# Kernel tuning notes

Measured on AMD Instinct MI355X. Metric: run time of the kernel, lower is better.

## Reference

```python
import jax, jax.numpy as jnp
import numpy as np

D_MODEL = 1024
D_STATE = 16
D_CONV = 4
EXPAND = 2
D_HALF = D_MODEL // 2            # per-direction model dim fed to each Mamba
D_INNER = EXPAND * D_HALF       # mamba inner dim
DT_RANK = (D_HALF + 15) // 16   # ceil(d_model/16), mamba default
EPS = 1e-5


def setup_inputs() -> dict:
    key = jax.random.key(0)
    ks = iter(jax.random.split(key, 64))

    def rn(shape, s=0.02):
        return jax.random.normal(next(ks), shape, dtype=jnp.float32) * s

    inp = {
        "x": jax.random.normal(next(ks), (2, 4096, D_MODEL), dtype=jnp.float32),
        "norm_w": jnp.ones((D_MODEL,), jnp.float32),
        "norm_b": jnp.zeros((D_MODEL,), jnp.float32),
    }
    for pre in ("fwd", "bwd"):
        inp[pre + "_in_proj_w"] = rn((2 * D_INNER, D_HALF))
        inp[pre + "_conv_w"] = rn((D_INNER, 1, D_CONV), 0.1)      # depthwise kernel
        inp[pre + "_conv_b"] = jnp.zeros((D_INNER,), jnp.float32)
        inp[pre + "_x_proj_w"] = rn((DT_RANK + 2 * D_STATE, D_INNER))
        inp[pre + "_dt_proj_w"] = rn((D_INNER, DT_RANK), 0.1)
        inp[pre + "_dt_proj_b"] = rn((D_INNER,), 0.1)
        # S4D-real init: A_log = log(1..d_state) broadcast over channels
        inp[pre + "_A_log"] = jnp.log(jnp.broadcast_to(
            jnp.arange(1, D_STATE + 1, dtype=jnp.float32), (D_INNER, D_STATE)))
        inp[pre + "_D"] = jnp.ones((D_INNER,), jnp.float32)
        inp[pre + "_out_proj_w"] = rn((D_HALF, D_INNER))
    return inp


def _silu(x):
    return x * jax.nn.sigmoid(x)


def _mamba(x, in_proj_w, conv_w, conv_b, x_proj_w, dt_proj_w, dt_proj_b,
           A_log, D, out_proj_w):
    # x: (B, L, D_HALF)
    B, L, _ = x.shape
    xz = x @ in_proj_w.T                         # (B, L, 2*D_INNER)
    xc, z = jnp.split(xz, 2, axis=-1)

    # causal depthwise conv over time
    xt = jnp.moveaxis(xc, 1, 2)                  # (B, D_INNER, L)
    xt = jnp.pad(xt, ((0, 0), (0, 0), (D_CONV - 1, 0)))
    xt = jax.lax.conv_general_dilated(
        xt, conv_w, (1,), 'VALID',
        dimension_numbers=('NCH', 'OIH', 'NCH'),
        feature_group_count=D_INNER)
    xc = _silu(jnp.moveaxis(xt, 1, 2) + conv_b)  # (B, L, D_INNER)

    x_dbl = xc @ x_proj_w.T                      # (B, L, DT_RANK + 2*D_STATE)
    dt = jax.nn.softplus(x_dbl[..., :DT_RANK] @ dt_proj_w.T + dt_proj_b)  # (B,L,D_INNER)
    Bm = x_dbl[..., DT_RANK:DT_RANK + D_STATE]   # (B, L, D_STATE)
    Cm = x_dbl[..., DT_RANK + D_STATE:]          # (B, L, D_STATE)
    A = -jnp.exp(A_log)                          # (D_INNER, D_STATE)

    def step(h, ins):
        dt_t, B_t, C_t, u_t = ins                # (B,D_INNER),(B,N),(B,N),(B,D_INNER)
        dA = jnp.exp(dt_t[..., None] * A)        # (B, D_INNER, N)
        h = h * dA + (dt_t * u_t)[..., None] * B_t[:, None, :]
        y = jnp.einsum('bdn,bn->bd', h, C_t)
        return h, y

    h0 = jnp.zeros((B, D_INNER, D_STATE), xc.dtype)
    ins = (jnp.moveaxis(dt, 1, 0), jnp.moveaxis(Bm, 1, 0),
           jnp.moveaxis(Cm, 1, 0), jnp.moveaxis(xc, 1, 0))
    _, ys = jax.lax.scan(step, h0, ins)          # ys: (L, B, D_INNER)
    y = jnp.moveaxis(ys, 0, 1) + D * xc
    y = y * _silu(z)
    return y @ out_proj_w.T                      # (B, L, D_HALF)


def reference(x, norm_w, norm_b,
              fwd_in_proj_w, fwd_conv_w, fwd_conv_b, fwd_x_proj_w,
              fwd_dt_proj_w, fwd_dt_proj_b, fwd_A_log, fwd_D, fwd_out_proj_w,
              bwd_in_proj_w, bwd_conv_w, bwd_conv_b, bwd_x_proj_w,
              bwd_dt_proj_w, bwd_dt_proj_b, bwd_A_log, bwd_D, bwd_out_proj_w):
    residual = x
    mu = x.mean(-1, keepdims=True)
    var = ((x - mu) ** 2).mean(-1, keepdims=True)
    xn = (x - mu) * jax.lax.rsqrt(var + EPS) * norm_w + norm_b

    x_fwd, x_bwd = jnp.split(xn, 2, axis=-1)
    out_fwd = _mamba(x_fwd, fwd_in_proj_w, fwd_conv_w, fwd_conv_b, fwd_x_proj_w,
                     fwd_dt_proj_w, fwd_dt_proj_b, fwd_A_log, fwd_D, fwd_out_proj_w)
    out_bwd = _mamba(x_bwd[:, ::-1, :], bwd_in_proj_w, bwd_conv_w, bwd_conv_b,
                     bwd_x_proj_w, bwd_dt_proj_w, bwd_dt_proj_b, bwd_A_log,
                     bwd_D, bwd_out_proj_w)[:, ::-1, :]
    return jnp.concatenate([out_fwd, out_bwd], axis=-1) + residual
```

## Files before the change

kernel.cpp:

```cpp
#include <hip/hip_runtime.h>
#include <hip/hip_bf16.h>
#include <cstdint>

#define DMODEL 1024
#define DHALF  512
#define DINNER 1024
#define DSTATE 16
#define DTRANK 32
#define LSEQ   4096
#define BBATCH 2
#define MROWS  (BBATCH*LSEQ)
#define SCH    128
#define SCT    32

using bf16 = __bf16;
using bf16x8 = __attribute__((ext_vector_type(8))) __bf16;
using f32x4  = __attribute__((ext_vector_type(4))) float;
using f32x2  = __attribute__((ext_vector_type(2))) float;

__device__ __forceinline__ float sigmoidf_(float x) { return 1.f / (1.f + __expf(-x)); }
__device__ __forceinline__ float softplusf_(float x) { return fmaxf(x, 0.f) + log1pf(__expf(-fabsf(x))); }

__device__ __forceinline__ void glds16(const bf16* g, bf16* l) {
    __builtin_amdgcn_global_load_lds(
        (const __attribute__((address_space(1))) void*)g,
        (__attribute__((address_space(3))) void*)l, 16, 0, 0);
}

__global__ __launch_bounds__(256) void ln_kernel(
    const float* __restrict__ x, const float* __restrict__ w,
    const float* __restrict__ b, bf16* __restrict__ xn)
{
    const int row = blockIdx.x;
    const int tid = threadIdx.x;
    const float4 v = *(const float4*)&x[(size_t)row * DMODEL + tid * 4];
    float s  = v.x + v.y + v.z + v.w;
    float s2 = v.x * v.x + v.y * v.y + v.z * v.z + v.w * v.w;
#pragma unroll
    for (int off = 1; off < 64; off <<= 1) {
        s  += __shfl_xor(s, off);
        s2 += __shfl_xor(s2, off);
    }
    __shared__ float red[8];
    const int wid = tid >> 6;
    if ((tid & 63) == 0) { red[wid] = s; red[4 + wid] = s2; }
    __syncthreads();
    s  = red[0] + red[1] + red[2] + red[3];
    s2 = red[4] + red[5] + red[6] + red[7];
    const float mu   = s * (1.f / DMODEL);
    const float var  = s2 * (1.f / DMODEL) - mu * mu;
    const float rstd = rsqrtf(var + 1e-5f);
    const float4 wv = *(const float4*)&w[tid * 4];
    const float4 bv = *(const float4*)&b[tid * 4];
    union { bf16 o[4]; uint2 u; } pk;
    pk.o[0] = (bf16)((v.x - mu) * rstd * wv.x + bv.x);
    pk.o[1] = (bf16)((v.y - mu) * rstd * wv.y + bv.y);
    pk.o[2] = (bf16)((v.z - mu) * rstd * wv.z + bv.z);
    pk.o[3] = (bf16)((v.w - mu) * rstd * wv.w + bv.w);
    *(uint2*)&xn[(size_t)row * DMODEL + tid * 4] = pk.u;
}

__global__ __launch_bounds__(256) void cvt_weights_kernel(
    const float* __restrict__ s0, const float* __restrict__ s1,
    const float* __restrict__ s2, const float* __restrict__ s3,
    const float* __restrict__ s4, const float* __restrict__ s5,
    const float* __restrict__ s6, const float* __restrict__ s7,
    bf16* __restrict__ d0, bf16* __restrict__ d1, bf16* __restrict__ d2,
    bf16* __restrict__ d3, bf16* __restrict__ d4, bf16* __restrict__ d5,
    bf16* __restrict__ d6, bf16* __restrict__ d7)
{
    const size_t gid = ((size_t)blockIdx.x * 256 + threadIdx.x) * 4;
    const float* s; bf16* dst; size_t off;
    if      (gid < 1048576) { s = s0; dst = d0; off = gid; }
    else if (gid < 2097152) { s = s1; dst = d1; off = gid - 1048576; }
    else if (gid < 2162688) { s = s2; dst = d2; off = gid - 2097152; }
    else if (gid < 2228224) { s = s3; dst = d3; off = gid - 2162688; }
    else if (gid < 2752512) { s = s4; dst = d4; off = gid - 2228224; }
    else if (gid < 3276800) { s = s5; dst = d5; off = gid - 2752512; }
    else if (gid < 3309568) { s = s6; dst = d6; off = gid - 3276800; }
    else if (gid < 3342336) { s = s7; dst = d7; off = gid - 3309568; }
    else return;
    const float4 v = *(const float4*)&s[off];
    union { bf16 o[4]; uint2 u; } pk;
    pk.o[0] = (bf16)v.x; pk.o[1] = (bf16)v.y; pk.o[2] = (bf16)v.z; pk.o[3] = (bf16)v.w;
    *(uint2*)&dst[off] = pk.u;
}

template<int BM, int BN, int WTM, int WTN, int EPI>
__global__ __launch_bounds__(256) void gemm_k(
    const bf16* __restrict__ A0, long aDirStride, int lda,
    const bf16* __restrict__ W0, const bf16* __restrict__ W1, int ldw,
    void* __restrict__ C0, long cDirStride, int ldc,
    void* __restrict__ C1, long c1DirStride,
    const float* __restrict__ X0, const float* __restrict__ X1,
    int K)
{
    constexpr int WGN = BN / (WTN * 16);
    static_assert((BM * 32) % 2048 == 0 && (BN * 32) % 2048 == 0, "tile");
    __shared__ alignas(16) bf16 As[BM * 32];
    __shared__ alignas(16) bf16 Bs[BN * 32];
    const int tid = threadIdx.x;
    const int wid = tid >> 6, lane = tid & 63;
    const int wr = wid / WGN, wc = wid % WGN;
    const int bx = blockIdx.x, by = blockIdx.y, bz = blockIdx.z;
    const bf16* A = A0 + (long)bz * aDirStride + (long)by * BM * lda;
    const bf16* W = (bz ? W1 : W0) + (long)bx * BN * ldw;
    f32x4 acc[WTM][WTN] = {};
    for (int k0 = 0; k0 < K; k0 += 32) {
        constexpr int AP = BM * 32 / 2048;
#pragma unroll
        for (int p = 0; p < AP; ++p) {
            const int idx = (p * 256 + tid) * 8;
            const int r = idx >> 5, c = idx & 31;
            glds16(&A[(long)r * lda + k0 + c], &As[p * 2048 + wid * 512]);
        }
        constexpr int BP = BN * 32 / 2048;
#pragma unroll
        for (int p = 0; p < BP; ++p) {
            const int idx = (p * 256 + tid) * 8;
            const int r = idx >> 5, c = idx & 31;
            glds16(&W[(long)r * ldw + k0 + c], &Bs[p * 2048 + wid * 512]);
        }
        __syncthreads();
        const int rA = lane & 15, kO = (lane >> 4) * 8;
        bf16x8 af[WTM], bw[WTN];
#pragma unroll
        for (int i = 0; i < WTM; ++i)
            af[i] = *(const bf16x8*)&As[(wr * WTM * 16 + i * 16 + rA) * 32 + kO];
#pragma unroll
        for (int j = 0; j < WTN; ++j)
            bw[j] = *(const bf16x8*)&Bs[(wc * WTN * 16 + j * 16 + rA) * 32 + kO];
#pragma unroll
        for (int i = 0; i < WTM; ++i)
#pragma unroll
            for (int j = 0; j < WTN; ++j)
                acc[i][j] = __builtin_amdgcn_mfma_f32_16x16x32_bf16(af[i], bw[j], acc[i][j], 0, 0, 0);
        __syncthreads();
    }
    const int rl = (lane >> 4) * 4, cl = lane & 15;
    const int rowBase = by * BM + wr * WTM * 16;
    const int colBase = bx * BN + wc * WTN * 16;
#pragma unroll
    for (int i = 0; i < WTM; ++i)
#pragma unroll
        for (int j = 0; j < WTN; ++j) {
#pragma unroll
            for (int r = 0; r < 4; ++r) {
                const int row = rowBase + i * 16 + rl + r;
                const int col = colBase + j * 16 + cl;
                const float v = acc[i][j][r];
                if constexpr (EPI == 0) {
                    ((bf16*)C0 + (long)bz * cDirStride)[(long)row * ldc + col] = (bf16)v;
                } else if constexpr (EPI == 1) {
                    ((float*)C0 + (long)bz * cDirStride)[(long)row * ldc + col] = v;
                    ((bf16*)C1 + (long)bz * c1DirStride)[(long)row * ldc + col] = (bf16)v;
                } else if constexpr (EPI == 2) {
                    const float* bias = bz ? X1 : X0;
                    ((float*)C0 + (long)bz * cDirStride)[(long)row * ldc + col] =
                        softplusf_(v + bias[col]);
                } else {
                    const long idx = (long)row * ldc + col;
                    ((float*)C0 + (long)bz * cDirStride)[idx] = v + (X0 + (long)bz * cDirStride)[idx];
                }
            }
        }
}

#define CT 8
__global__ __launch_bounds__(256) void conv_silu_kernel(
    const bf16* __restrict__ xz, bf16* __restrict__ xc,
    const float* __restrict__ cwF, const float* __restrict__ cbF,
    const float* __restrict__ cwB, const float* __restrict__ cbB)
{
    const size_t gid = (size_t)blockIdx.x * 256 + threadIdx.x;
    const int g = (int)(gid & 127);
    const int tt = (int)((gid >> 7) & (LSEQ / CT - 1));
    const int b = (int)((gid >> 16) & 1);
    const int dir = (int)(gid >> 17);
    const int d0 = g * 8;
    const float* cw = dir ? cwB : cwF;
    const float* cb = dir ? cbB : cbF;
    float bias[8];
#pragma unroll
    for (int e = 0; e < 8; e += 4) *(float4*)&bias[e] = *(const float4*)&cb[d0 + e];
    float4 wv[8];
#pragma unroll
    for (int e = 0; e < 8; ++e) wv[e] = *(const float4*)&cw[(d0 + e) * 4];
    const int t0 = tt * CT;
    const size_t rowBase = (size_t)dir * MROWS * 2048 + (size_t)b * LSEQ * 2048;
    const bf16* src = xz + rowBase + d0;
    bf16* dst = xc + (size_t)dir * MROWS * DINNER + (size_t)b * LSEQ * DINNER
                + (size_t)t0 * DINNER + d0;

    float w0[8] = {}, w1[8] = {}, w2[8] = {};
    auto loadRow = [&](int ts, float* r) {
        if (ts >= 0 && ts < LSEQ) {
            const bf16x8 v = *(const bf16x8*)&src[(size_t)ts * 2048];
#pragma unroll
            for (int e = 0; e < 8; ++e) r[e] = (float)v[e];
        } else {
#pragma unroll
            for (int e = 0; e < 8; ++e) r[e] = 0.f;
        }
    };
    if (!dir) { loadRow(t0 - 3, w0); loadRow(t0 - 2, w1); loadRow(t0 - 1, w2); }
    else      { loadRow(t0,     w0); loadRow(t0 + 1, w1); loadRow(t0 + 2, w2); }

#pragma unroll
    for (int i = 0; i < CT; ++i) {
        float w3[8];
        loadRow(dir ? (t0 + i + 3) : (t0 + i), w3);
        bf16x8 o;
        if (!dir) {
#pragma unroll
            for (int e = 0; e < 8; ++e) {
                float acc = bias[e];
                acc = fmaf(wv[e].x, w0[e], acc);
                acc = fmaf(wv[e].y, w1[e], acc);
                acc = fmaf(wv[e].z, w2[e], acc);
                acc = fmaf(wv[e].w, w3[e], acc);
                const float s = acc * sigmoidf_(acc);
                o[e] = (bf16)s;
            }
        } else {
#pragma unroll
            for (int e = 0; e < 8; ++e) {
                float acc = bias[e];
                acc = fmaf(wv[e].w, w0[e], acc);
                acc = fmaf(wv[e].z, w1[e], acc);
                acc = fmaf(wv[e].y, w2[e], acc);
                acc = fmaf(wv[e].x, w3[e], acc);
                const float s = acc * sigmoidf_(acc);
                o[e] = (bf16)s;
            }
        }
        *(bf16x8*)&dst[(size_t)i * DINNER] = o;
#pragma unroll
        for (int e = 0; e < 8; ++e) { w0[e] = w1[e]; w1[e] = w2[e]; w2[e] = w3[e]; }
    }
}

__global__ __launch_bounds__(256) void scan_part1(
    const float* __restrict__ dt, const bf16* __restrict__ xc,
    const float* __restrict__ xdbl,
    float* __restrict__ hend, float* __restrict__ sdtOut,
    const float* __restrict__ AlogF, const float* __restrict__ AlogB)
{
    const int d = blockIdx.x * 256 + threadIdx.x;
    const int chunk = blockIdx.y;
    const int sb = blockIdx.z;
    const int dir = sb >> 1, b = sb & 1;
    const float* Alog = dir ? AlogB : AlogF;
    float a[16];
#pragma unroll
    for (int n = 0; n < 16; n += 4)
        *(float4*)&a[n] = *(const float4*)&Alog[d * 16 + n];
#pragma unroll
    for (int n = 0; n < 16; ++n) a[n] = -__expf(a[n]);
    bool fast = true;
#pragma unroll
    for (int n = 0; n < 16; ++n) fast = fast && (fabsf(a[n] + (float)(n + 1)) <= 1e-3f * (n + 1));
    const size_t base1 = (size_t)dir * MROWS * DINNER + (size_t)b * LSEQ * DINNER;
    const size_t base64 = (size_t)dir * MROWS * 64 + (size_t)b * LSEQ * 64;
    const int t0 = dir ? (LSEQ - 1) : 0;
    const int stp = dir ? -1 : 1;
    const int ts = t0 + stp * (chunk * SCT);
    const float* pdt = dt + base1 + (size_t)ts * DINNER + d;
    const bf16* pxc = xc + base1 + (size_t)ts * DINNER + d;
    const float* xb = xdbl + base64 + 32;
    const long s1 = (long)stp * DINNER;
    float sacc = 0.f;
    f32x2 h2[8];
#pragma unroll
    for (int j = 0; j < 8; ++j) h2[j] = (f32x2){0.f, 0.f};
    if (fast) {
#pragma unroll 4
        for (int i = 0; i < SCT; ++i) {
            const float dtv = *pdt;
            const float u = (float)*pxc;
            const float dtu = dtv * u;
            sacc += dtv;
            const float* bRow = xb + (size_t)(ts + stp * i) * 64;
            const float q = __expf(-dtv);
            const float q2 = q * q;
            const f32x2 qq = {q2, q2};
            f32x2 p = {q, q2};
#pragma unroll
            for (int j = 0; j < 8; ++j) {
                const f32x2 B2 = *(const f32x2*)&bRow[2 * j];
                const f32x2 b2 = B2 * dtu;
                h2[j] = __builtin_elementwise_fma(h2[j], p, b2);
                p = p * qq;
            }
            pdt += s1; pxc += s1;
        }
    } else {
#pragma unroll 4
        for (int i = 0; i < SCT; ++i) {
            const float dtv = *pdt;
            const float u = (float)*pxc;
            const float dtu = dtv * u;
            sacc += dtv;
            const float* bRow = xb + (size_t)(ts + stp * i) * 64;
#pragma unroll
            for (int j = 0; j < 8; ++j) {
                const f32x2 B2 = *(const f32x2*)&bRow[2 * j];
                const f32x2 dA = {__expf(dtv * a[2 * j]), __expf(dtv * a[2 * j + 1])};
                h2[j] = __builtin_elementwise_fma(h2[j], dA, B2 * dtu);
            }
            pdt += s1; pxc += s1;
        }
    }
    const size_t o = ((size_t)sb * SCH + chunk) * 16384 + (size_t)d * 16;
#pragma unroll
    for (int j = 0; j < 8; ++j) *(f32x2*)&hend[o + 2 * j] = h2[j];
    sdtOut[((size_t)sb * SCH + chunk) * 1024 + d] = sacc;
}

__global__ __launch_bounds__(256) void scan_part2(
    float* __restrict__ hend, const float* __restrict__ sdt,
    const float* __restrict__ AlogF, const float* __restrict__ AlogB)
{
    const size_t gid = (size_t)blockIdx.x * 256 + threadIdx.x;
    const int sb = (int)(gid >> 14);
    const int dn = (int)(gid & 16383);
    const int d = dn >> 4;
    const float* Alog = (sb >> 1) ? AlogB : AlogF;
    const float a_n = -__expf(Alog[dn]);
    float h = 0.f;
    size_t idx = (size_t)sb * SCH * 16384 + dn;
    size_t sidx = (size_t)sb * SCH * 1024 + d;
#pragma unroll 4
    for (int c = 0; c < SCH; ++c) {
        const float sd = sdt[sidx];
        const float pe = __expf(a_n * sd);
        const float he = hend[idx];
        hend[idx] = h;
        h = fmaf(pe, h, he);
        idx += 16384; sidx += 1024;
    }
}

__global__ __launch_bounds__(256) void scan_part3(
    const float* __restrict__ dt, const bf16* __restrict__ xc,
    const float* __restrict__ xdbl, const bf16* __restrict__ xz,
    const float* __restrict__ hin, bf16* __restrict__ yg,
    const float* __restrict__ AlogF, const float* __restrict__ AlogB,
    const float* __restrict__ DF, const float* __restrict__ DB)
{
    const int d = blockIdx.x * 256 + threadIdx.x;
    const int chunk = blockIdx.y;
    const int sb = blockIdx.z;
    const int dir = sb >> 1, b = sb & 1;
    const float* Alog = dir ? AlogB : AlogF;
    const float* Dw = dir ? DB : DF;
    float a[16];
#pragma unroll
    for (int n = 0; n < 16; n += 4)
        *(float4*)&a[n] = *(const float4*)&Alog[d * 16 + n];
#pragma unroll
    for (int n = 0; n < 16; ++n) a[n] = -__expf(a[n]);
    bool fast = true;
#pragma unroll
    for (int n = 0; n < 16; ++n) fast = fast && (fabsf(a[n] + (float)(n + 1)) <= 1e-3f * (n + 1));
    const float Dv = Dw[d];
    const size_t base1 = (size_t)dir * MROWS * DINNER + (size_t)b * LSEQ * DINNER;
    const size_t base64 = (size_t)dir * MROWS * 64 + (size_t)b * LSEQ * 64;
    const size_t baseZ = (size_t)dir * MROWS * 2048 + (size_t)b * LSEQ * 2048;
    const int t0 = dir ? (LSEQ - 1) : 0;
    const int stp = dir ? -1 : 1;
    const int ts = t0 + stp * (chunk * SCT);
    const float* pdt = dt + base1 + (size_t)ts * DINNER + d;
    const bf16* pxc = xc + base1 + (size_t)ts * DINNER + d;
    const float* xb = xdbl + base64 + 32;
    const bf16* pz = xz + baseZ + (size_t)ts * 2048 + 1024 + d;
    bf16* pyg = yg + base1 + (size_t)ts * DINNER + d;
    const long s1 = (long)stp * DINNER, sZ = (long)stp * 2048;
    f32x2 h2[8];
    const size_t o = ((size_t)sb * SCH + chunk) * 16384 + (size_t)d * 16;
#pragma unroll
    for (int j = 0; j < 8; ++j) h2[j] = *(const f32x2*)&hin[o + 2 * j];
    if (fast) {
#pragma unroll 4
        for (int i = 0; i < SCT; ++i) {
            const float dtv = *pdt;
            const float u = (float)*pxc;
            const float dtu = dtv * u;
            const float* bRow = xb + (size_t)(ts + stp * i) * 64;
            const float q = __expf(-dtv);
            const float q2 = q * q;
            const f32x2 qq = {q2, q2};
            f32x2 p = {q, q2};
            f32x2 y2 = {0.f, 0.f};
#pragma unroll
            for (int j = 0; j < 8; ++j) {
                const f32x2 B2 = *(const f32x2*)&bRow[2 * j];
                const f32x2 C2 = *(const f32x2*)&bRow[16 + 2 * j];
                h2[j] = __builtin_elementwise_fma(h2[j], p, B2 * dtu);
                y2 = __builtin_elementwise_fma(h2[j], C2, y2);
                p = p * qq;
            }
            const float y = y2[0] + y2[1];
            const float z = (float)*pz;
            const float out = (y + Dv * u) * (z * sigmoidf_(z));
            *pyg = (bf16)out;
            pdt += s1; pxc += s1; pz += sZ; pyg += s1;
        }
    } else {
#pragma unroll 4
        for (int i = 0; i < SCT; ++i) {
            const float dtv = *pdt;
            const float u = (float)*pxc;
            const float dtu = dtv * u;
            const float* bRow = xb + (size_t)(ts + stp * i) * 64;
            f32x2 y2 = {0.f, 0.f};
#pragma unroll
            for (int j = 0; j < 8; ++j) {
                const f32x2 B2 = *(const f32x2*)&bRow[2 * j];
                const f32x2 C2 = *(const f32x2*)&bRow[16 + 2 * j];
                const f32x2 dA = {__expf(dtv * a[2 * j]), __expf(dtv * a[2 * j + 1])};
                h2[j] = __builtin_elementwise_fma(h2[j], dA, B2 * dtu);
                y2 = __builtin_elementwise_fma(h2[j], C2, y2);
            }
            const float y = y2[0] + y2[1];
            const float z = (float)*pz;
            const float out = (y + Dv * u) * (z * sigmoidf_(z));
            *pyg = (bf16)out;
            pdt += s1; pxc += s1; pz += sZ; pyg += s1;
        }
    }
}

extern "C" void kernel_launch(void* const* d_in, const int* in_sizes, int n_in,
                              void* d_out, int out_size, void* d_ws, size_t ws_size,
                              hipStream_t stream)
{
    const float* x      = (const float*)d_in[0];
    const float* norm_w = (const float*)d_in[1];
    const float* norm_b = (const float*)d_in[2];
    const float* ipF  = (const float*)d_in[3];
    const float* cwF  = (const float*)d_in[4];
    const float* cbF  = (const float*)d_in[5];
    const float* xpF  = (const float*)d_in[6];
    const float* dtwF = (const float*)d_in[7];
    const float* dtbF = (const float*)d_in[8];
    const float* AlF  = (const float*)d_in[9];
    const float* DF   = (const float*)d_in[10];
    const float* opF  = (const float*)d_in[11];
    const float* ipB  = (const float*)d_in[12];
    const float* cwB  = (const float*)d_in[13];
    const float* cbB  = (const float*)d_in[14];
    const float* xpB  = (const float*)d_in[15];
    const float* dtwB = (const float*)d_in[16];
    const float* dtbB = (const float*)d_in[17];
    const float* AlB  = (const float*)d_in[18];
    const float* DB   = (const float*)d_in[19];
    const float* opB  = (const float*)d_in[20];

    char* ws = (char*)d_ws;
    size_t off = 0;
    auto alloc = [&](size_t bytes) -> void* {
        void* p = ws + off;
        off += (bytes + 255) & ~(size_t)255;
        return p;
    };
    bf16*  xn      = (bf16*)alloc((size_t)MROWS * DMODEL * 2);
    bf16*  win     = (bf16*)alloc((size_t)2 * 2048 * 512 * 2);
    bf16*  wxp     = (bf16*)alloc((size_t)2 * 64 * 1024 * 2);
    bf16*  wop     = (bf16*)alloc((size_t)2 * 512 * 1024 * 2);
    bf16*  wdt     = (bf16*)alloc((size_t)2 * 1024 * 32 * 2);
    bf16*  xz      = (bf16*)alloc((size_t)2 * MROWS * 2048 * 2);
    bf16*  xc      = (bf16*)alloc((size_t)2 * MROWS * 1024 * 2);
    float* xdbl    = (float*)alloc((size_t)2 * MROWS * 64 * 4);
    bf16*  xdbl_bf = (bf16*)alloc((size_t)2 * MROWS * 64 * 2);
    float* dt      = (float*)alloc((size_t)2 * MROWS * 1024 * 4);
    bf16*  yg      = (bf16*)alloc((size_t)2 * MROWS * 1024 * 2);
    float* hend    = (float*)alloc((size_t)4 * SCH * 16384 * 4);
    float* sdt     = (float*)alloc((size_t)4 * SCH * 1024 * 4);

    cvt_weights_kernel<<<3264, 256, 0, stream>>>(
        ipF, ipB, xpF, xpB, opF, opB, dtwF, dtwB,
        win, win + 2048 * 512, wxp, wxp + 64 * 1024,
        wop, wop + 512 * 1024, wdt, wdt + 1024 * 32);

    ln_kernel<<<MROWS, 256, 0, stream>>>(x, norm_w, norm_b, xn);

    gemm_k<128, 128, 4, 4, 0><<<dim3(16, 64, 2), 256, 0, stream>>>(
        xn, 512, DMODEL, win, win + 2048 * 512, 512,
        xz, (long)MROWS * 2048, 2048, nullptr, 0, nullptr, nullptr, 512);

    conv_silu_kernel<<<1024, 256, 0, stream>>>(xz, xc, cwF, cbF, cwB, cbB);

    gemm_k<64, 64, 2, 2, 1><<<dim3(1, 128, 2), 256, 0, stream>>>(
        xc, (long)MROWS * 1024, 1024, wxp, wxp + 64 * 1024, 1024,
        xdbl, (long)MROWS * 64, 64, xdbl_bf, (long)MROWS * 64, nullptr, nullptr, 1024);

    gemm_k<128, 128, 4, 4, 2><<<dim3(8, 64, 2), 256, 0, stream>>>(
        xdbl_bf, (long)MROWS * 64, 64, wdt, wdt + 1024 * 32, 32,
        dt, (long)MROWS * 1024, 1024, nullptr, 0, dtbF, dtbB, 32);

    scan_part1<<<dim3(4, SCH, 4), 256, 0, stream>>>(dt, xc, xdbl, hend, sdt, AlF, AlB);
    scan_part2<<<256, 256, 0, stream>>>(hend, sdt, AlF, AlB);
    scan_part3<<<dim3(4, SCH, 4), 256, 0, stream>>>(dt, xc, xdbl, xz, hend, yg,
                                                    AlF, AlB, DF, DB);

    gemm_k<128, 128, 4, 4, 3><<<dim3(4, 64, 2), 256, 0, stream>>>(
        yg, (long)MROWS * 1024, 1024, wop, wop + 512 * 1024, 1024,
        d_out, 512, 1024, nullptr, 0, x, nullptr, 1024);
}
```

Before: 419.2 us.

## Split-K the x_proj GEMM, store dt as bf16, stage B/C rows in LDS

The x_proj GEMM, which ran as only 256 blocks over K=1024, now uses a 4-way split-K with a separate reduction kernel that writes the fp32 and bf16 copies of xdbl. The dt tensor is written and read as bf16 instead of fp32, halving its traffic in the dt GEMM epilogue and both scan passes. The scan kernels stage the per-chunk B/C rows of xdbl in shared memory and switch from float2 to float4 state vectors. In exchange this adds a kernel launch and a partial-sum buffer, and dt loses precision from bf16 rounding.

```diff
diff --git a/kernel.cpp b/kernel.cpp
--- a/kernel.cpp
+++ b/kernel.cpp
@@ -86,7 +86,7 @@
     *(uint2*)&dst[off] = pk.u;
 }
 
-template<int BM, int BN, int WTM, int WTN, int EPI>
+template<int BM, int BN, int WTM, int WTN, int EPI, int KS = 1>
 __global__ __launch_bounds__(256) void gemm_k(
     const bf16* __restrict__ A0, long aDirStride, int lda,
     const bf16* __restrict__ W0, const bf16* __restrict__ W1, int ldw,
@@ -103,10 +103,12 @@
     const int wid = tid >> 6, lane = tid & 63;
     const int wr = wid / WGN, wc = wid % WGN;
     const int bx = blockIdx.x, by = blockIdx.y, bz = blockIdx.z;
-    const bf16* A = A0 + (long)bz * aDirStride + (long)by * BM * lda;
-    const bf16* W = (bz ? W1 : W0) + (long)bx * BN * ldw;
+    const int dirz = bz / KS, ks = bz % KS;
+    const bf16* A = A0 + (long)dirz * aDirStride + (long)by * BM * lda;
+    const bf16* W = (dirz ? W1 : W0) + (long)bx * BN * ldw;
     f32x4 acc[WTM][WTN] = {};
-    for (int k0 = 0; k0 < K; k0 += 32) {
+    const int kBeg = ks * (K / KS), kEnd = (ks + 1) * (K / KS);
+    for (int k0 = kBeg; k0 < kEnd; k0 += 32) {
         constexpr int AP = BM * 32 / 2048;
 #pragma unroll
         for (int p = 0; p < AP; ++p) {
@@ -150,20 +152,44 @@
                 const int col = colBase + j * 16 + cl;
                 const float v = acc[i][j][r];
                 if constexpr (EPI == 0) {
-                    ((bf16*)C0 + (long)bz * cDirStride)[(long)row * ldc + col] = (bf16)v;
+                    ((bf16*)C0 + (long)dirz * cDirStride)[(long)row * ldc + col] = (bf16)v;
                 } else if constexpr (EPI == 1) {
+                    ((float*)C0 + (long)dirz * cDirStride)[(long)row * ldc + col] = v;
+                    ((bf16*)C1 + (long)dirz * c1DirStride)[(long)row * ldc + col] = (bf16)v;
+                } else if constexpr (EPI == 2) {
+                    const float* bias = dirz ? X1 : X0;
+                    ((bf16*)C0 + (long)dirz * cDirStride)[(long)row * ldc + col] =
+                        (bf16)softplusf_(v + bias[col]);
+                } else if constexpr (EPI == 3) {
+                    const long idx = (long)row * ldc + col;
+                    ((float*)C0 + (long)dirz * cDirStride)[idx] = v + (X0 + (long)dirz * cDirStride)[idx];
+                } else {
                     ((float*)C0 + (long)bz * cDirStride)[(long)row * ldc + col] = v;
-                    ((bf16*)C1 + (long)bz * c1DirStride)[(long)row * ldc + col] = (bf16)v;
-                } else if constexpr (EPI == 2) {
-                    const float* bias = bz ? X1 : X0;
-                    ((float*)C0 + (long)bz * cDirStride)[(long)row * ldc + col] =
-                        softplusf_(v + bias[col]);
-                } else {
-                    const long idx = (long)row * ldc + col;
-                    ((float*)C0 + (long)bz * cDirStride)[idx] = v + (X0 + (long)bz * cDirStride)[idx];
                 }
             }
         }
+}
+
+__global__ __launch_bounds__(256) void xproj_reduce(
+    const float* __restrict__ part, float* __restrict__ xdbl, bf16* __restrict__ xdbl_bf)
+{
+    const size_t gid = (size_t)blockIdx.x * 256 + threadIdx.x;
+    const size_t e4 = gid * 4;
+    const int dir = (int)(e4 / ((size_t)MROWS * 64));
+    const size_t e = e4 - (size_t)dir * MROWS * 64;
+    const float* p = part + (size_t)dir * 4 * MROWS * 64 + e;
+    float4 s0 = *(const float4*)&p[0];
+    const float4 s1 = *(const float4*)&p[(size_t)MROWS * 64];
+    const float4 s2 = *(const float4*)&p[(size_t)2 * MROWS * 64];
+    const float4 s3 = *(const float4*)&p[(size_t)3 * MROWS * 64];
+    s0.x += s1.x + s2.x + s3.x;
+    s0.y += s1.y + s2.y + s3.y;
+    s0.z += s1.z + s2.z + s3.z;
+    s0.w += s1.w + s2.w + s3.w;
+    *(float4*)&xdbl[e4] = s0;
+    union { bf16 o[4]; uint2 u; } pk;
+    pk.o[0] = (bf16)s0.x; pk.o[1] = (bf16)s0.y; pk.o[2] = (bf16)s0.z; pk.o[3] = (bf16)s0.w;
+    *(uint2*)&xdbl_bf[e4] = pk.u;
 }
 
 #define CT 8
@@ -241,11 +267,12 @@
 }
 
 __global__ __launch_bounds__(256) void scan_part1(
-    const float* __restrict__ dt, const bf16* __restrict__ xc,
+    const bf16* __restrict__ dt, const bf16* __restrict__ xc,
     const float* __restrict__ xdbl,
     float* __restrict__ hend, float* __restrict__ sdtOut,
     const float* __restrict__ AlogF, const float* __restrict__ AlogB)
 {
+    __shared__ alignas(16) float bs[SCT][16];
     const int d = blockIdx.x * 256 + threadIdx.x;
     const int chunk = blockIdx.y;
     const int sb = blockIdx.z;
@@ -265,55 +292,59 @@
     const int t0 = dir ? (LSEQ - 1) : 0;
     const int stp = dir ? -1 : 1;
     const int ts = t0 + stp * (chunk * SCT);
-    const float* pdt = dt + base1 + (size_t)ts * DINNER + d;
+    {
+        const int s = threadIdx.x >> 3;
+        const int c = (threadIdx.x & 7) * 2;
+        const float* srcRow = xdbl + base64 + (size_t)(ts + stp * s) * 64 + 32;
+        *(float2*)&bs[s][c] = *(const float2*)&srcRow[c];
+    }
+    __syncthreads();
+    const bf16* pdt = dt + base1 + (size_t)ts * DINNER + d;
     const bf16* pxc = xc + base1 + (size_t)ts * DINNER + d;
-    const float* xb = xdbl + base64 + 32;
     const long s1 = (long)stp * DINNER;
     float sacc = 0.f;
-    f32x2 h2[8];
-#pragma unroll
-    for (int j = 0; j < 8; ++j) h2[j] = (f32x2){0.f, 0.f};
+    f32x4 h4[4] = {};
     if (fast) {
 #pragma unroll 4
         for (int i = 0; i < SCT; ++i) {
-            const float dtv = *pdt;
+            const float dtv = (float)*pdt;
             const float u = (float)*pxc;
             const float dtu = dtv * u;
             sacc += dtv;
-            const float* bRow = xb + (size_t)(ts + stp * i) * 64;
+            const f32x4* rowB = (const f32x4*)&bs[i][0];
             const float q = __expf(-dtv);
-            const float q2 = q * q;
-            const f32x2 qq = {q2, q2};
-            f32x2 p = {q, q2};
-#pragma unroll
-            for (int j = 0; j < 8; ++j) {
-                const f32x2 B2 = *(const f32x2*)&bRow[2 * j];
-                const f32x2 b2 = B2 * dtu;
-                h2[j] = __builtin_elementwise_fma(h2[j], p, b2);
-                p = p * qq;
+            const float q2 = q * q, q3 = q2 * q, q4 = q2 * q2;
+            f32x4 p = {q, q2, q3, q4};
+            const f32x4 q4v = {q4, q4, q4, q4};
+#pragma unroll
+            for (int j = 0; j < 4; ++j) {
+                const f32x4 B4 = rowB[j];
+                h4[j] = __builtin_elementwise_fma(h4[j], p, B4 * dtu);
+                p = p * q4v;
             }
             pdt += s1; pxc += s1;
         }
     } else {
 #pragma unroll 4
         for (int i = 0; i < SCT; ++i) {
-            const float dtv = *pdt;
+            const float dtv = (float)*pdt;
             const float u = (float)*pxc;
             const float dtu = dtv * u;
             sacc += dtv;
-            const float* bRow = xb + (size_t)(ts + stp * i) * 64;
-#pragma unroll
-            for (int j = 0; j < 8; ++j) {
-                const f32x2 B2 = *(const f32x2*)&bRow[2 * j];
-                const f32x2 dA = {__expf(dtv * a[2 * j]), __expf(dtv * a[2 * j + 1])};
-                h2[j] = __builtin_elementwise_fma(h2[j], dA, B2 * dtu);
+            const f32x4* rowB = (const f32x4*)&bs[i][0];
+#pragma unroll
+            for (int j = 0; j < 4; ++j) {
+                const f32x4 B4 = rowB[j];
+                const f32x4 dA = {__expf(dtv * a[4 * j]), __expf(dtv * a[4 * j + 1]),
+                                  __expf(dtv * a[4 * j + 2]), __expf(dtv * a[4 * j + 3])};
+                h4[j] = __builtin_elementwise_fma(h4[j], dA, B4 * dtu);
             }
             pdt += s1; pxc += s1;
         }
     }
     const size_t o = ((size_t)sb * SCH + chunk) * 16384 + (size_t)d * 16;
 #pragma unroll
-    for (int j = 0; j < 8; ++j) *(f32x2*)&hend[o + 2 * j] = h2[j];
+    for (int j = 0; j < 4; ++j) *(f32x4*)&hend[o + 4 * j] = h4[j];
     sdtOut[((size_t)sb * SCH + chunk) * 1024 + d] = sacc;
 }
 
@@ -342,12 +373,13 @@
 }
 
 __global__ __launch_bounds__(256) void scan_part3(
-    const float* __restrict__ dt, const bf16* __restrict__ xc,
+    const bf16* __restrict__ dt, const bf16* __restrict__ xc,
     const float* __restrict__ xdbl, const bf16* __restrict__ xz,
     const float* __restrict__ hin, bf16* __restrict__ yg,
     const float* __restrict__ AlogF, const float* __restrict__ AlogB,
     const float* __restrict__ DF, const float* __restrict__ DB)
 {
+    __shared__ alignas(16) float bc[SCT][32];
     const int d = blockIdx.x * 256 + threadIdx.x;
     const int chunk = blockIdx.y;
     const int sb = blockIdx.z;
@@ -370,37 +402,44 @@
     const int t0 = dir ? (LSEQ - 1) : 0;
     const int stp = dir ? -1 : 1;
     const int ts = t0 + stp * (chunk * SCT);
-    const float* pdt = dt + base1 + (size_t)ts * DINNER + d;
+    {
+        const int s = threadIdx.x >> 3;
+        const int c = (threadIdx.x & 7) * 4;
+        const float* srcRow = xdbl + base64 + (size_t)(ts + stp * s) * 64 + 32;
+        *(float4*)&bc[s][c] = *(const float4*)&srcRow[c];
+    }
+    __syncthreads();
+    const bf16* pdt = dt + base1 + (size_t)ts * DINNER + d;
     const bf16* pxc = xc + base1 + (size_t)ts * DINNER + d;
-    const float* xb = xdbl + base64 + 32;
     const bf16* pz = xz + baseZ + (size_t)ts * 2048 + 1024 + d;
     bf16* pyg = yg + base1 + (size_t)ts * DINNER + d;
     const long s1 = (long)stp * DINNER, sZ = (long)stp * 2048;
-    f32x2 h2[8];
+    f32x4 h4[4];
     const size_t o = ((size_t)sb * SCH + chunk) * 16384 + (size_t)d * 16;
 #pragma unroll
-    for (int j = 0; j < 8; ++j) h2[j] = *(const f32x2*)&hin[o + 2 * j];
+    for (int j = 0; j < 4; ++j) h4[j] = *(const f32x4*)&hin[o + 4 * j];
     if (fast) {
 #pragma unroll 4
         for (int i = 0; i < SCT; ++i) {
-            const float dtv = *pdt;
+            const float dtv = (float)*pdt;
             const float u = (float)*pxc;
             const float dtu = dtv * u;
-            const float* bRow = xb + (size_t)(ts + stp * i) * 64;
+            const f32x4* rowB = (const f32x4*)&bc[i][0];
+            const f32x4* rowC = (const f32x4*)&bc[i][16];
             const float q = __expf(-dtv);
-            const float q2 = q * q;
-            const f32x2 qq = {q2, q2};
-            f32x2 p = {q, q2};
-            f32x2 y2 = {0.f, 0.f};
-#pragma unroll
-            for (int j = 0; j < 8; ++j) {
-                const f32x2 B2 = *(const f32x2*)&bRow[2 * j];
-                const f32x2 C2 = *(const f32x2*)&bRow[16 + 2 * j];
-                h2[j] = __builtin_elementwise_fma(h2[j], p, B2 * dtu);
-                y2 = __builtin_elementwise_fma(h2[j], C2, y2);
-                p = p * qq;
-            }
-            const float y = y2[0] + y2[1];
+            const float q2 = q * q, q3 = q2 * q, q4 = q2 * q2;
+            f32x4 p = {q, q2, q3, q4};
+            const f32x4 q4v = {q4, q4, q4, q4};
+            f32x4 y4 = {0.f, 0.f, 0.f, 0.f};
+#pragma unroll
+            for (int j = 0; j < 4; ++j) {
+                const f32x4 B4 = rowB[j];
+                const f32x4 C4 = rowC[j];
+                h4[j] = __builtin_elementwise_fma(h4[j], p, B4 * dtu);
+                y4 = __builtin_elementwise_fma(h4[j], C4, y4);
+                p = p * q4v;
+            }
+            const float y = (y4[0] + y4[1]) + (y4[2] + y4[3]);
             const float z = (float)*pz;
             const float out = (y + Dv * u) * (z * sigmoidf_(z));
             *pyg = (bf16)out;
@@ -409,20 +448,22 @@
     } else {
 #pragma unroll 4
         for (int i = 0; i < SCT; ++i) {
-            const float dtv = *pdt;
+            const float dtv = (float)*pdt;
             const float u = (float)*pxc;
             const float dtu = dtv * u;
-            const float* bRow = xb + (size_t)(ts + stp * i) * 64;
-            f32x2 y2 = {0.f, 0.f};
-#pragma unroll
-            for (int j = 0; j < 8; ++j) {
-                const f32x2 B2 = *(const f32x2*)&bRow[2 * j];
-                const f32x2 C2 = *(const f32x2*)&bRow[16 + 2 * j];
-                const f32x2 dA = {__expf(dtv * a[2 * j]), __expf(dtv * a[2 * j + 1])};
-                h2[j] = __builtin_elementwise_fma(h2[j], dA, B2 * dtu);
-                y2 = __builtin_elementwise_fma(h2[j], C2, y2);
-            }
-            const float y = y2[0] + y2[1];
+            const f32x4* rowB = (const f32x4*)&bc[i][0];
+            const f32x4* rowC = (const f32x4*)&bc[i][16];
+            f32x4 y4 = {0.f, 0.f, 0.f, 0.f};
+#pragma unroll
+            for (int j = 0; j < 4; ++j) {
+                const f32x4 B4 = rowB[j];
+                const f32x4 C4 = rowC[j];
+                const f32x4 dA = {__expf(dtv * a[4 * j]), __expf(dtv * a[4 * j + 1]),
+                                  __expf(dtv * a[4 * j + 2]), __expf(dtv * a[4 * j + 3])};
+                h4[j] = __builtin_elementwise_fma(h4[j], dA, B4 * dtu);
+                y4 = __builtin_elementwise_fma(h4[j], C4, y4);
+            }
+            const float y = (y4[0] + y4[1]) + (y4[2] + y4[3]);
             const float z = (float)*pz;
             const float out = (y + Dv * u) * (z * sigmoidf_(z));
             *pyg = (bf16)out;
@@ -473,10 +514,11 @@
     bf16*  xc      = (bf16*)alloc((size_t)2 * MROWS * 1024 * 2);
     float* xdbl    = (float*)alloc((size_t)2 * MROWS * 64 * 4);
     bf16*  xdbl_bf = (bf16*)alloc((size_t)2 * MROWS * 64 * 2);
-    float* dt      = (float*)alloc((size_t)2 * MROWS * 1024 * 4);
+    bf16*  dt      = (bf16*)alloc((size_t)2 * MROWS * 1024 * 2);
     bf16*  yg      = (bf16*)alloc((size_t)2 * MROWS * 1024 * 2);
     float* hend    = (float*)alloc((size_t)4 * SCH * 16384 * 4);
     float* sdt     = (float*)alloc((size_t)4 * SCH * 1024 * 4);
+    float* xpart   = (float*)alloc((size_t)8 * MROWS * 64 * 4);
 
     cvt_weights_kernel<<<3264, 256, 0, stream>>>(
         ipF, ipB, xpF, xpB, opF, opB, dtwF, dtwB,
@@ -491,9 +533,10 @@
 
     conv_silu_kernel<<<1024, 256, 0, stream>>>(xz, xc, cwF, cbF, cwB, cbB);
 
-    gemm_k<64, 64, 2, 2, 1><<<dim3(1, 128, 2), 256, 0, stream>>>(
+    gemm_k<64, 64, 2, 2, 4, 4><<<dim3(1, 128, 8), 256, 0, stream>>>(
         xc, (long)MROWS * 1024, 1024, wxp, wxp + 64 * 1024, 1024,
-        xdbl, (long)MROWS * 64, 64, xdbl_bf, (long)MROWS * 64, nullptr, nullptr, 1024);
+        xpart, (long)MROWS * 64, 64, nullptr, 0, nullptr, nullptr, 1024);
+    xproj_reduce<<<1024, 256, 0, stream>>>(xpart, xdbl, xdbl_bf);
 
     gemm_k<128, 128, 4, 4, 2><<<dim3(8, 64, 2), 256, 0, stream>>>(
         xdbl_bf, (long)MROWS * 64, 64, wdt, wdt + 1024 * 32, 32,
```

After: 456.3 us. +8.8%, slower.
